# Optimization experiments

Measured on AMD Instinct MI355X. Metric: run time of the kernel, lower is better.

Reference implementation:

```python
import jax, jax.numpy as jnp
import numpy as np

N_LAYERS = 2
N_QUBITS = 2


def _ry(t):
    c, s = jnp.cos(t / 2), jnp.sin(t / 2)
    m = jnp.stack([jnp.stack([c, -s], -1), jnp.stack([s, c], -1)], -2)
    return m.astype(jnp.complex64)


def _rx(t):
    c = jnp.cos(t / 2).astype(jnp.complex64)
    s = (-1j) * jnp.sin(t / 2).astype(jnp.complex64)
    return jnp.stack([jnp.stack([c, s], -1), jnp.stack([s, c], -1)], -2)


def _rz(t):
    e = jnp.exp(-0.5j * t.astype(jnp.complex64))
    z = jnp.zeros_like(e)
    return jnp.stack([jnp.stack([e, z], -1), jnp.stack([z, jnp.conj(e)], -1)], -2)


def _apply_w0(G, s):
    # gate on wire 0 (most significant); s: [N,2,2] indexed [n, q0, q1]
    if G.ndim == 2:
        G = G[None]
    return jnp.matmul(G, s)


def _apply_w1(G, s):
    # gate on wire 1: contract last index with G
    if G.ndim == 2:
        G = G[None]
    return jnp.matmul(s, jnp.swapaxes(G, -1, -2))


def _qnn_batched(enc, qw):
    # enc: [N,2] float angles; qw: [2,2,3] trainable angles.
    # Batched 2-qubit statevector simulation, state shape [N,2,2] (q0,q1).
    N = enc.shape[0]
    s = jnp.zeros((N, 2, 2), jnp.complex64).at[:, 0, 0].set(1.0)
    # data encoding: RY(enc_i) on wire i
    s = _apply_w0(_ry(enc[:, 0]), s)
    s = _apply_w1(_ry(enc[:, 1]), s)
    for l in range(N_LAYERS):
        # RX then RY then RZ on each qubit => fused single-qubit gate RZ@RY@RX
        g0 = _rz(qw[l, 0, 2]) @ _ry(qw[l, 0, 1]) @ _rx(qw[l, 0, 0])
        g1 = _rz(qw[l, 1, 2]) @ _ry(qw[l, 1, 1]) @ _rx(qw[l, 1, 0])
        s = _apply_w0(g0, s)
        s = _apply_w1(g1, s)
        # CNOT(control=0, target=1): flip q1 where q0 == 1
        s = s.at[:, 1, :].set(s[:, 1, ::-1])
    p = (s * jnp.conj(s)).real  # probabilities [N,2,2]
    z0 = (p[:, 0, :] - p[:, 1, :]).sum(-1)
    z1 = (p[:, :, 0] - p[:, :, 1]).sum(-1)
    return jnp.stack([z0, z1], -1)  # [N,2]


def _mlp(x, w1, b1, w2, b2, w3, b3):
    h = jnp.tanh(x @ w1 + b1)
    h = jnp.tanh(h @ w2 + b2)
    return h @ w3 + b3


def setup_inputs() -> dict:
    key = jax.random.key(0)
    ks = jax.random.split(key, 15)
    N = 1_000_000
    W = 32

    def rn(k, shape, scale):
        return (scale * jax.random.normal(k, shape)).astype(jnp.float32)

    return {
        "x": rn(ks[0], (N, 1), 1.0),
        "pre_w1": rn(ks[1], (1, W), 1.0),
        "pre_b1": rn(ks[2], (W,), 0.1),
        "pre_w2": rn(ks[3], (W, W), 1.0 / np.sqrt(W)),
        "pre_b2": rn(ks[4], (W,), 0.1),
        "pre_w3": rn(ks[5], (W, 2), 1.0 / np.sqrt(W)),
        "pre_b3": rn(ks[6], (2,), 0.1),
        "q_weights": rn(ks[7], (N_LAYERS, N_QUBITS, 3), 0.1),
        "post_w1": rn(ks[8], (2, W), 1.0 / np.sqrt(2)),
        "post_b1": rn(ks[9], (W,), 0.1),
        "post_w2": rn(ks[10], (W, W), 1.0 / np.sqrt(W)),
        "post_b2": rn(ks[11], (W,), 0.1),
        "post_w3": rn(ks[12], (W, 1), 1.0 / np.sqrt(W)),
        "post_b3": rn(ks[13], (1,), 0.1),
    }


def reference(x, pre_w1, pre_b1, pre_w2, pre_b2, pre_w3, pre_b3, q_weights,
              post_w1, post_b1, post_w2, post_b2, post_w3, post_b3):
    q = _mlp(x, pre_w1, pre_b1, pre_w2, pre_b2, pre_w3, pre_b3)        # [N,2]
    qhat = _qnn_batched(q, q_weights)                                  # [N,2]
    u = _mlp(qhat, post_w1, post_b1, post_w2, post_b2, post_w3, post_b3)  # [N,1]
    return u
```

## Files before the change

kernel.cpp:

```cpp
#include <hip/hip_runtime.h>
#include <math.h>
#include <stdint.h>


typedef __attribute__((ext_vector_type(8))) short short8;
typedef __attribute__((ext_vector_type(4))) float f32x4;

union Frag { uint32_t u[4]; short8 s; };

__device__ __forceinline__ float fast_tanh(float x) {
    float e = __builtin_amdgcn_exp2f(x * 2.8853900817779268f);
    return fmaf(-2.0f, __builtin_amdgcn_rcpf(e + 1.0f), 1.0f);
}

__device__ __forceinline__ void split8(const float h[8], uint32_t hi[4], uint32_t lo[4]) {
    #pragma unroll
    for (int p = 0; p < 4; ++p) {
        uint32_t u0 = __float_as_uint(h[2*p])   & 0xFFFF0000u;
        uint32_t u1 = __float_as_uint(h[2*p+1]) & 0xFFFF0000u;
        float l0 = h[2*p]   - __uint_as_float(u0);
        float l1 = h[2*p+1] - __uint_as_float(u1);
        uint32_t v0 = __float_as_uint(l0) & 0xFFFF0000u;
        uint32_t v1 = __float_as_uint(l1) & 0xFFFF0000u;
        hi[p] = (u0 >> 16) | u1;
        lo[p] = (v0 >> 16) | v1;
    }
}

struct cplx { float re, im; };
__device__ __forceinline__ cplx cmul(cplx a, cplx b) {
    return { a.re * b.re - a.im * b.im, a.re * b.im + a.im * b.re };
}
__device__ __forceinline__ cplx cadd(cplx a, cplx b) {
    return { a.re + b.re, a.im + b.im };
}

__global__ void qcpinn_setup(const float* __restrict__ qw,
                             const float* __restrict__ pw2,
                             const float* __restrict__ ow2,
                             float* __restrict__ ws) {
    const int lane = threadIdx.x & 63;
    const int s = lane & 15, gg = lane >> 4;
    uint32_t* wsu = (uint32_t*)ws;

    #pragma unroll
    for (int m = 0; m < 2; ++m) {
        const float* W = m ? ow2 : pw2;
        #pragma unroll
        for (int r = 0; r < 2; ++r) {
            float v[8];
            #pragma unroll
            for (int j = 0; j < 8; ++j)
                v[j] = W[(gg * 8 + j) * 32 + (r * 16 + s)];
            uint32_t hi[4], lo[4];
            split8(v, hi, lo);
            int bh = 32 + ((m * 4 + r * 2 + 0) * 64 + lane) * 4;
            int bl = 32 + ((m * 4 + r * 2 + 1) * 64 + lane) * 4;
            #pragma unroll
            for (int p = 0; p < 4; ++p) { wsu[bh + p] = hi[p]; wsu[bl + p] = lo[p]; }
        }
    }

    if (threadIdx.x == 0) {
        cplx U[16];
        for (int i = 0; i < 16; ++i) U[i] = {0.f, 0.f};
        U[0].re = U[5].re = U[10].re = U[15].re = 1.f;

        for (int l = 0; l < 2; ++l) {
            cplx g[2][4];
            for (int w = 0; w < 2; ++w) {
                float a = qw[l * 6 + w * 3 + 0];
                float b = qw[l * 6 + w * 3 + 1];
                float c = qw[l * 6 + w * 3 + 2];
                float sa, ca, sb, cb, sc, cc;
                __sincosf(0.5f * a, &sa, &ca);
                __sincosf(0.5f * b, &sb, &cb);
                __sincosf(0.5f * c, &sc, &cc);
                cplx RX[4] = {{ca, 0.f}, {0.f, -sa}, {0.f, -sa}, {ca, 0.f}};
                cplx RY[4] = {{cb, 0.f}, {-sb, 0.f}, {sb, 0.f}, {cb, 0.f}};
                cplx RZ[4] = {{cc, -sc}, {0.f, 0.f}, {0.f, 0.f}, {cc, sc}};
                cplx T[4];
                for (int i2 = 0; i2 < 2; ++i2)
                    for (int j2 = 0; j2 < 2; ++j2) {
                        cplx acc = {0.f, 0.f};
                        for (int k2 = 0; k2 < 2; ++k2)
                            acc = cadd(acc, cmul(RY[i2 * 2 + k2], RX[k2 * 2 + j2]));
                        T[i2 * 2 + j2] = acc;
                    }
                for (int i2 = 0; i2 < 2; ++i2)
                    for (int j2 = 0; j2 < 2; ++j2) {
                        cplx acc = {0.f, 0.f};
                        for (int k2 = 0; k2 < 2; ++k2)
                            acc = cadd(acc, cmul(RZ[i2 * 2 + k2], T[k2 * 2 + j2]));
                        g[w][i2 * 2 + j2] = acc;
                    }
            }
            cplx L[16];
            for (int i4 = 0; i4 < 4; ++i4) {
                int si = (i4 == 2) ? 3 : (i4 == 3) ? 2 : i4;
                for (int j4 = 0; j4 < 4; ++j4)
                    L[i4 * 4 + j4] = cmul(g[1][(si & 1) * 2 + (j4 & 1)],
                                          g[0][(si >> 1) * 2 + (j4 >> 1)]);
            }
            cplx Un[16];
            for (int i4 = 0; i4 < 4; ++i4)
                for (int j4 = 0; j4 < 4; ++j4) {
                    cplx acc = {0.f, 0.f};
                    for (int k4 = 0; k4 < 4; ++k4)
                        acc = cadd(acc, cmul(L[i4 * 4 + k4], U[k4 * 4 + j4]));
                    Un[i4 * 4 + j4] = acc;
                }
            for (int i = 0; i < 16; ++i) U[i] = Un[i];
        }
        for (int i = 0; i < 16; ++i) { ws[i] = U[i].re; ws[16 + i] = U[i].im; }
    }
}

#define NT 4
__global__ __launch_bounds__(256, 4) void qcpinn_main(
    const float* __restrict__ x,
    const float* __restrict__ pw1, const float* __restrict__ pb1,
    const float* __restrict__ pb2, const float* __restrict__ pw3,
    const float* __restrict__ pb3,
    const float* __restrict__ ws,
    const float* __restrict__ ow1, const float* __restrict__ ob1,
    const float* __restrict__ ob2, const float* __restrict__ ow3,
    const float* __restrict__ ob3,
    float* __restrict__ out, int N)
{
    const int lane = threadIdx.x & 63;
    const int wid  = threadIdx.x >> 6;
    const int s    = lane & 15;
    const int g    = lane >> 4;
    const int base = (blockIdx.x * 4 + wid) * (NT * 16);

    const Frag* fragp = (const Frag*)(ws + 32);

    float xv[NT];
    #pragma unroll
    for (int t = 0; t < NT; ++t) {
        int idx = base + t * 16 + s;
        xv[t] = (idx < N) ? x[idx] : 0.f;
    }

    f32x4 w1a = *(const f32x4*)(pw1 + g * 8);
    f32x4 w1b = *(const f32x4*)(pw1 + g * 8 + 4);
    f32x4 b1a = *(const f32x4*)(pb1 + g * 8);
    f32x4 b1b = *(const f32x4*)(pb1 + g * 8 + 4);
    Frag A0h = fragp[0 * 64 + lane];
    Frag A0l = fragp[1 * 64 + lane];
    Frag A1h = fragp[2 * 64 + lane];
    Frag A1l = fragp[3 * 64 + lane];
    f32x4 pb2a = *(const f32x4*)(pb2 + g * 4);
    f32x4 pb2b = *(const f32x4*)(pb2 + 16 + g * 4);
    f32x4 w3a = *(const f32x4*)(pw3 + g * 8);
    f32x4 w3b = *(const f32x4*)(pw3 + g * 8 + 4);
    f32x4 w3c = *(const f32x4*)(pw3 + 32 + g * 8);
    f32x4 w3d = *(const f32x4*)(pw3 + 32 + g * 8 + 4);
    const float bq0 = pb3[0], bq1 = pb3[1];
    f32x4 Ure = *(const f32x4*)(ws + g * 4);
    f32x4 Uim = *(const f32x4*)(ws + 16 + g * 4);
    const float sgn0 = (g & 2) ? -1.f : 1.f;
    const float sgn1 = (g & 1) ? -1.f : 1.f;

    float z0[NT], z1[NT];
    #pragma unroll
    for (int t = 0; t < NT; ++t) {
        float h[8];
        #pragma unroll
        for (int j = 0; j < 4; ++j) {
            h[j]     = fast_tanh(fmaf(xv[t], w1a[j], b1a[j]));
            h[4 + j] = fast_tanh(fmaf(xv[t], w1b[j], b1b[j]));
        }
        Frag Bh, Bl;
        split8(h, Bh.u, Bl.u);

        f32x4 C0 = {0.f, 0.f, 0.f, 0.f};
        f32x4 C1 = {0.f, 0.f, 0.f, 0.f};
        C0 = __builtin_amdgcn_mfma_f32_16x16x32_bf16(A0h.s, Bh.s, C0, 0, 0, 0);
        C0 = __builtin_amdgcn_mfma_f32_16x16x32_bf16(A0h.s, Bl.s, C0, 0, 0, 0);
        C0 = __builtin_amdgcn_mfma_f32_16x16x32_bf16(A0l.s, Bh.s, C0, 0, 0, 0);
        C1 = __builtin_amdgcn_mfma_f32_16x16x32_bf16(A1h.s, Bh.s, C1, 0, 0, 0);
        C1 = __builtin_amdgcn_mfma_f32_16x16x32_bf16(A1h.s, Bl.s, C1, 0, 0, 0);
        C1 = __builtin_amdgcn_mfma_f32_16x16x32_bf16(A1l.s, Bh.s, C1, 0, 0, 0);

        float h2[8];
        #pragma unroll
        for (int i = 0; i < 4; ++i) {
            h2[i]     = fast_tanh(C0[i] + pb2a[i]);
            h2[4 + i] = fast_tanh(C1[i] + pb2b[i]);
        }

        float q0 = 0.f, q1 = 0.f;
        q0 = fmaf(h2[0], w3a[0], q0); q1 = fmaf(h2[0], w3a[1], q1);
        q0 = fmaf(h2[1], w3a[2], q0); q1 = fmaf(h2[1], w3a[3], q1);
        q0 = fmaf(h2[2], w3b[0], q0); q1 = fmaf(h2[2], w3b[1], q1);
        q0 = fmaf(h2[3], w3b[2], q0); q1 = fmaf(h2[3], w3b[3], q1);
        q0 = fmaf(h2[4], w3c[0], q0); q1 = fmaf(h2[4], w3c[1], q1);
        q0 = fmaf(h2[5], w3c[2], q0); q1 = fmaf(h2[5], w3c[3], q1);
        q0 = fmaf(h2[6], w3d[0], q0); q1 = fmaf(h2[6], w3d[1], q1);
        q0 = fmaf(h2[7], w3d[2], q0); q1 = fmaf(h2[7], w3d[3], q1);
        q0 += __shfl_xor(q0, 16); q0 += __shfl_xor(q0, 32); q0 += bq0;
        q1 += __shfl_xor(q1, 16); q1 += __shfl_xor(q1, 32); q1 += bq1;

        float s0, c0, s1, c1;
        __sincosf(0.5f * q0, &s0, &c0);
        __sincosf(0.5f * q1, &s1, &c1);
        float e0 = c0 * c1, e1 = c0 * s1, e2 = s0 * c1, e3 = s0 * s1;
        float re = fmaf(Ure[0], e0, fmaf(Ure[1], e1, fmaf(Ure[2], e2, Ure[3] * e3)));
        float im = fmaf(Uim[0], e0, fmaf(Uim[1], e1, fmaf(Uim[2], e2, Uim[3] * e3)));
        float p  = fmaf(re, re, im * im);
        float t0 = sgn0 * p, t1 = sgn1 * p;
        t0 += __shfl_xor(t0, 16); t0 += __shfl_xor(t0, 32);
        t1 += __shfl_xor(t1, 16); t1 += __shfl_xor(t1, 32);
        z0[t] = t0; z1[t] = t1;
    }

    f32x4 oa   = *(const f32x4*)(ow1 + g * 8);
    f32x4 oa2  = *(const f32x4*)(ow1 + g * 8 + 4);
    f32x4 obv  = *(const f32x4*)(ow1 + 32 + g * 8);
    f32x4 ob2v = *(const f32x4*)(ow1 + 32 + g * 8 + 4);
    f32x4 obb  = *(const f32x4*)(ob1 + g * 8);
    f32x4 obb2 = *(const f32x4*)(ob1 + g * 8 + 4);
    Frag P0h = fragp[4 * 64 + lane];
    Frag P0l = fragp[5 * 64 + lane];
    Frag P1h = fragp[6 * 64 + lane];
    Frag P1l = fragp[7 * 64 + lane];
    f32x4 ob2a = *(const f32x4*)(ob2 + g * 4);
    f32x4 ob2b = *(const f32x4*)(ob2 + 16 + g * 4);
    f32x4 w3o0 = *(const f32x4*)(ow3 + g * 4);
    f32x4 w3o1 = *(const f32x4*)(ow3 + 16 + g * 4);
    const float bo = ob3[0];

    #pragma unroll
    for (int t = 0; t < NT; ++t) {
        float h[8];
        #pragma unroll
        for (int j = 0; j < 4; ++j) {
            h[j]     = fast_tanh(fmaf(z0[t], oa[j],  fmaf(z1[t], obv[j],  obb[j])));
            h[4 + j] = fast_tanh(fmaf(z0[t], oa2[j], fmaf(z1[t], ob2v[j], obb2[j])));
        }
        Frag Bh, Bl;
        split8(h, Bh.u, Bl.u);

        f32x4 C0 = {0.f, 0.f, 0.f, 0.f};
        f32x4 C1 = {0.f, 0.f, 0.f, 0.f};
        C0 = __builtin_amdgcn_mfma_f32_16x16x32_bf16(P0h.s, Bh.s, C0, 0, 0, 0);
        C0 = __builtin_amdgcn_mfma_f32_16x16x32_bf16(P0h.s, Bl.s, C0, 0, 0, 0);
        C0 = __builtin_amdgcn_mfma_f32_16x16x32_bf16(P0l.s, Bh.s, C0, 0, 0, 0);
        C1 = __builtin_amdgcn_mfma_f32_16x16x32_bf16(P1h.s, Bh.s, C1, 0, 0, 0);
        C1 = __builtin_amdgcn_mfma_f32_16x16x32_bf16(P1h.s, Bl.s, C1, 0, 0, 0);
        C1 = __builtin_amdgcn_mfma_f32_16x16x32_bf16(P1l.s, Bh.s, C1, 0, 0, 0);

        float u = 0.f;
        #pragma unroll
        for (int i = 0; i < 4; ++i) {
            float ha = fast_tanh(C0[i] + ob2a[i]);
            float hb = fast_tanh(C1[i] + ob2b[i]);
            u = fmaf(ha, w3o0[i], u);
            u = fmaf(hb, w3o1[i], u);
        }
        u += __shfl_xor(u, 16);
        u += __shfl_xor(u, 32);
        u += bo;
        int idx = base + t * 16 + s;
        if (g == 0 && idx < N) out[idx] = u;
    }
}

extern "C" void kernel_launch(void* const* d_in, const int* in_sizes, int n_in,
                              void* d_out, int out_size, void* d_ws, size_t ws_size,
                              hipStream_t stream) {
    const float* x   = (const float*)d_in[0];
    const float* pw1 = (const float*)d_in[1];
    const float* pb1 = (const float*)d_in[2];
    const float* pw2 = (const float*)d_in[3];
    const float* pb2 = (const float*)d_in[4];
    const float* pw3 = (const float*)d_in[5];
    const float* pb3 = (const float*)d_in[6];
    const float* qw  = (const float*)d_in[7];
    const float* ow1 = (const float*)d_in[8];
    const float* ob1 = (const float*)d_in[9];
    const float* ow2 = (const float*)d_in[10];
    const float* ob2 = (const float*)d_in[11];
    const float* ow3 = (const float*)d_in[12];
    const float* ob3 = (const float*)d_in[13];
    float* out = (float*)d_out;
    float* ws  = (float*)d_ws;

    const int N = in_sizes[0];

    qcpinn_setup<<<1, 64, 0, stream>>>(qw, pw2, ow2, ws);

    const int grid = (N + 255) / 256;
    qcpinn_main<<<grid, 256, 0, stream>>>(
        x, pw1, pb1, pb2, pw3, pb3, ws,
        ow1, ob1, ob2, ow3, ob3, out, N);
}
```

Baseline: 126.3 us.

## Rewrite tanh as scaled sigmoid, fold constants into weights, stage params in LDS

Rewrites each tanh as 1-2*sigmoid and folds the scale factors, column sums and signs into the preprocessed weights and biases in the setup kernel. The main kernel then needs one exp and one rcp per activation with no extra FMA. The activation B operand drops from a hi/lo bf16 split to a single rounded bf16, which cuts MFMAs from 6 to 4 per layer and removes the split work. The two stages are fused into one loop. Parameters are staged through LDS, and the output store is coalesced so each lane writes one value. The cost is lower precision in the activations and an extra block-wide LDS copy and barrier.

New measurement: 118.8 us. 1.06x faster.

```diff
diff --git a/kernel.cpp b/kernel.cpp
--- a/kernel.cpp
+++ b/kernel.cpp
@@ -1,4 +1,5 @@
 #include <hip/hip_runtime.h>
+#include <hip/hip_bf16.h>
 #include <math.h>
 #include <stdint.h>
 
@@ -8,9 +9,30 @@
 
 union Frag { uint32_t u[4]; short8 s; };
 
-__device__ __forceinline__ float fast_tanh(float x) {
-    float e = __builtin_amdgcn_exp2f(x * 2.8853900817779268f);
-    return fmaf(-2.0f, __builtin_amdgcn_rcpf(e + 1.0f), 1.0f);
+#define KT 2.8853900817779268f
+
+#define L_FRAG 0
+#define L_U    2048
+#define L_W1   2080
+#define L_B1   2112
+#define L_BH2  2144
+#define L_W3   2176
+#define L_OW1  2240
+#define L_OB1  2304
+#define L_BH2P 2336
+#define L_OW3  2368
+#define L_SC   2400
+#define L_TOT  2416
+
+__device__ __forceinline__ float sig_act(float y) {
+    return __builtin_amdgcn_rcpf(__builtin_amdgcn_exp2f(y) + 1.0f);
+}
+
+__device__ __forceinline__ uint32_t pk_bf16(float a, float b) {
+    union { __hip_bfloat162 h; uint32_t u; } cv;
+    cv.h.x = __float2bfloat16(a);
+    cv.h.y = __float2bfloat16(b);
+    return cv.u;
 }
 
 __device__ __forceinline__ void split8(const float h[8], uint32_t hi[4], uint32_t lo[4]) {
@@ -35,10 +57,16 @@
     return { a.re + b.re, a.im + b.im };
 }
 
-__global__ void qcpinn_setup(const float* __restrict__ qw,
-                             const float* __restrict__ pw2,
-                             const float* __restrict__ ow2,
-                             float* __restrict__ ws) {
+__global__ void qcpinn_setup(
+    const float* __restrict__ pw1, const float* __restrict__ pb1,
+    const float* __restrict__ pw2, const float* __restrict__ pb2,
+    const float* __restrict__ pw3, const float* __restrict__ pb3,
+    const float* __restrict__ qw,
+    const float* __restrict__ ow1, const float* __restrict__ ob1,
+    const float* __restrict__ ow2, const float* __restrict__ ob2,
+    const float* __restrict__ ow3, const float* __restrict__ ob3,
+    float* __restrict__ ws)
+{
     const int lane = threadIdx.x & 63;
     const int s = lane & 15, gg = lane >> 4;
     uint32_t* wsu = (uint32_t*)ws;
@@ -51,21 +79,47 @@
             float v[8];
             #pragma unroll
             for (int j = 0; j < 8; ++j)
-                v[j] = W[(gg * 8 + j) * 32 + (r * 16 + s)];
+                v[j] = -2.0f * KT * W[(gg * 8 + j) * 32 + (r * 16 + s)];
             uint32_t hi[4], lo[4];
             split8(v, hi, lo);
-            int bh = 32 + ((m * 4 + r * 2 + 0) * 64 + lane) * 4;
-            int bl = 32 + ((m * 4 + r * 2 + 1) * 64 + lane) * 4;
+            int bh = L_FRAG + ((m * 4 + r * 2 + 0) * 256) + lane * 4;
+            int bl = L_FRAG + ((m * 4 + r * 2 + 1) * 256) + lane * 4;
             #pragma unroll
             for (int p = 0; p < 4; ++p) { wsu[bh + p] = hi[p]; wsu[bl + p] = lo[p]; }
         }
     }
 
-    if (threadIdx.x == 0) {
+    if (lane < 32) {
+        int j = lane;
+        float cs_p = 0.f, cs_o = 0.f;
+        for (int k = 0; k < 32; ++k) { cs_p += pw2[k * 32 + j]; cs_o += ow2[k * 32 + j]; }
+        ws[L_W1 + j]   = KT * pw1[j];
+        ws[L_B1 + j]   = KT * pb1[j];
+        ws[L_BH2 + j]  = KT * (pb2[j] + cs_p);
+        ws[L_OB1 + j]  = KT * ob1[j];
+        ws[L_BH2P + j] = KT * (ob2[j] + cs_o);
+        ws[L_OW3 + j]  = -2.f * ow3[j];
+        ws[L_W3 + j * 2]     = -pw3[j * 2];
+        ws[L_W3 + j * 2 + 1] = -pw3[j * 2 + 1];
+        float sg0 = (j & 16) ? -1.f : 1.f;
+        float sg1 = (j & 8)  ? -1.f : 1.f;
+        ws[L_OW1 + j]      = KT * sg0 * ow1[j];
+        ws[L_OW1 + 32 + j] = KT * sg1 * ow1[32 + j];
+    }
+
+    if (lane == 0) {
+        float cw0 = 0.f, cw1 = 0.f, co3 = 0.f;
+        for (int k = 0; k < 32; ++k) {
+            cw0 += pw3[k * 2]; cw1 += pw3[k * 2 + 1]; co3 += ow3[k];
+        }
+        ws[L_SC + 0] = 0.5f * (pb3[0] + cw0);
+        ws[L_SC + 1] = 0.5f * (pb3[1] + cw1);
+        ws[L_SC + 2] = ob3[0] + co3;
+        ws[L_SC + 3] = 0.f;
+
         cplx U[16];
         for (int i = 0; i < 16; ++i) U[i] = {0.f, 0.f};
         U[0].re = U[5].re = U[10].re = U[15].re = 1.f;
-
         for (int l = 0; l < 2; ++l) {
             cplx g[2][4];
             for (int w = 0; w < 2; ++w) {
@@ -112,29 +166,30 @@
                 }
             for (int i = 0; i < 16; ++i) U[i] = Un[i];
         }
-        for (int i = 0; i < 16; ++i) { ws[i] = U[i].re; ws[16 + i] = U[i].im; }
+        for (int i = 0; i < 16; ++i) { ws[L_U + i] = U[i].re; ws[L_U + 16 + i] = U[i].im; }
     }
 }
 
 #define NT 4
-__global__ __launch_bounds__(256, 4) void qcpinn_main(
-    const float* __restrict__ x,
-    const float* __restrict__ pw1, const float* __restrict__ pb1,
-    const float* __restrict__ pb2, const float* __restrict__ pw3,
-    const float* __restrict__ pb3,
-    const float* __restrict__ ws,
-    const float* __restrict__ ow1, const float* __restrict__ ob1,
-    const float* __restrict__ ob2, const float* __restrict__ ow3,
-    const float* __restrict__ ob3,
+__global__ __launch_bounds__(256) void qcpinn_main(
+    const float* __restrict__ x, const float* __restrict__ ws,
     float* __restrict__ out, int N)
 {
+    __shared__ float lds[L_TOT];
+    {
+        const float4* src = (const float4*)ws;
+        float4* dst = (float4*)lds;
+        for (int i = threadIdx.x; i < L_TOT / 4; i += 256) dst[i] = src[i];
+    }
+    __syncthreads();
+
     const int lane = threadIdx.x & 63;
     const int wid  = threadIdx.x >> 6;
     const int s    = lane & 15;
     const int g    = lane >> 4;
-    const int base = (blockIdx.x * 4 + wid) * (NT * 16);
-
-    const Frag* fragp = (const Frag*)(ws + 32);
+    const int base = (blockIdx.x * 4 + wid) * 64;
+
+    const Frag* frag = (const Frag*)(lds + L_FRAG);
 
     float xv[NT];
     #pragma unroll
@@ -143,129 +198,113 @@
         xv[t] = (idx < N) ? x[idx] : 0.f;
     }
 
-    f32x4 w1a = *(const f32x4*)(pw1 + g * 8);
-    f32x4 w1b = *(const f32x4*)(pw1 + g * 8 + 4);
-    f32x4 b1a = *(const f32x4*)(pb1 + g * 8);
-    f32x4 b1b = *(const f32x4*)(pb1 + g * 8 + 4);
-    Frag A0h = fragp[0 * 64 + lane];
-    Frag A0l = fragp[1 * 64 + lane];
-    Frag A1h = fragp[2 * 64 + lane];
-    Frag A1l = fragp[3 * 64 + lane];
-    f32x4 pb2a = *(const f32x4*)(pb2 + g * 4);
-    f32x4 pb2b = *(const f32x4*)(pb2 + 16 + g * 4);
-    f32x4 w3a = *(const f32x4*)(pw3 + g * 8);
-    f32x4 w3b = *(const f32x4*)(pw3 + g * 8 + 4);
-    f32x4 w3c = *(const f32x4*)(pw3 + 32 + g * 8);
-    f32x4 w3d = *(const f32x4*)(pw3 + 32 + g * 8 + 4);
-    const float bq0 = pb3[0], bq1 = pb3[1];
-    f32x4 Ure = *(const f32x4*)(ws + g * 4);
-    f32x4 Uim = *(const f32x4*)(ws + 16 + g * 4);
-    const float sgn0 = (g & 2) ? -1.f : 1.f;
-    const float sgn1 = (g & 1) ? -1.f : 1.f;
-
-    float z0[NT], z1[NT];
+    f32x4 w1a = *(const f32x4*)(lds + L_W1 + g * 8);
+    f32x4 w1b = *(const f32x4*)(lds + L_W1 + g * 8 + 4);
+    f32x4 b1a = *(const f32x4*)(lds + L_B1 + g * 8);
+    f32x4 b1b = *(const f32x4*)(lds + L_B1 + g * 8 + 4);
+    Frag A0h = frag[0 * 64 + lane], A0l = frag[1 * 64 + lane];
+    Frag A1h = frag[2 * 64 + lane], A1l = frag[3 * 64 + lane];
+    f32x4 bh2a = *(const f32x4*)(lds + L_BH2 + g * 4);
+    f32x4 bh2b = *(const f32x4*)(lds + L_BH2 + 16 + g * 4);
+    f32x4 w3a = *(const f32x4*)(lds + L_W3 + g * 8);
+    f32x4 w3b = *(const f32x4*)(lds + L_W3 + g * 8 + 4);
+    f32x4 w3c = *(const f32x4*)(lds + L_W3 + 32 + g * 8);
+    f32x4 w3d = *(const f32x4*)(lds + L_W3 + 32 + g * 8 + 4);
+    f32x4 Ure = *(const f32x4*)(lds + L_U + g * 4);
+    f32x4 Uim = *(const f32x4*)(lds + L_U + 16 + g * 4);
+    const float qb0 = lds[L_SC + 0], qb1 = lds[L_SC + 1], bo = lds[L_SC + 2];
+    f32x4 oa   = *(const f32x4*)(lds + L_OW1 + g * 8);
+    f32x4 oa2  = *(const f32x4*)(lds + L_OW1 + g * 8 + 4);
+    f32x4 obv  = *(const f32x4*)(lds + L_OW1 + 32 + g * 8);
+    f32x4 ob2v = *(const f32x4*)(lds + L_OW1 + 32 + g * 8 + 4);
+    f32x4 obb  = *(const f32x4*)(lds + L_OB1 + g * 8);
+    f32x4 obb2 = *(const f32x4*)(lds + L_OB1 + g * 8 + 4);
+    Frag P0h = frag[4 * 64 + lane], P0l = frag[5 * 64 + lane];
+    Frag P1h = frag[6 * 64 + lane], P1l = frag[7 * 64 + lane];
+    f32x4 bpa = *(const f32x4*)(lds + L_BH2P + g * 4);
+    f32x4 bpb = *(const f32x4*)(lds + L_BH2P + 16 + g * 4);
+    f32x4 w3o0 = *(const f32x4*)(lds + L_OW3 + g * 4);
+    f32x4 w3o1 = *(const f32x4*)(lds + L_OW3 + 16 + g * 4);
+
+    float uo[NT];
     #pragma unroll
     for (int t = 0; t < NT; ++t) {
-        float h[8];
+        float r1[8];
         #pragma unroll
         for (int j = 0; j < 4; ++j) {
-            h[j]     = fast_tanh(fmaf(xv[t], w1a[j], b1a[j]));
-            h[4 + j] = fast_tanh(fmaf(xv[t], w1b[j], b1b[j]));
-        }
-        Frag Bh, Bl;
-        split8(h, Bh.u, Bl.u);
-
-        f32x4 C0 = {0.f, 0.f, 0.f, 0.f};
-        f32x4 C1 = {0.f, 0.f, 0.f, 0.f};
-        C0 = __builtin_amdgcn_mfma_f32_16x16x32_bf16(A0h.s, Bh.s, C0, 0, 0, 0);
-        C0 = __builtin_amdgcn_mfma_f32_16x16x32_bf16(A0h.s, Bl.s, C0, 0, 0, 0);
-        C0 = __builtin_amdgcn_mfma_f32_16x16x32_bf16(A0l.s, Bh.s, C0, 0, 0, 0);
-        C1 = __builtin_amdgcn_mfma_f32_16x16x32_bf16(A1h.s, Bh.s, C1, 0, 0, 0);
-        C1 = __builtin_amdgcn_mfma_f32_16x16x32_bf16(A1h.s, Bl.s, C1, 0, 0, 0);
-        C1 = __builtin_amdgcn_mfma_f32_16x16x32_bf16(A1l.s, Bh.s, C1, 0, 0, 0);
-
-        float h2[8];
-        #pragma unroll
-        for (int i = 0; i < 4; ++i) {
-            h2[i]     = fast_tanh(C0[i] + pb2a[i]);
-            h2[4 + i] = fast_tanh(C1[i] + pb2b[i]);
-        }
-
-        float q0 = 0.f, q1 = 0.f;
-        q0 = fmaf(h2[0], w3a[0], q0); q1 = fmaf(h2[0], w3a[1], q1);
-        q0 = fmaf(h2[1], w3a[2], q0); q1 = fmaf(h2[1], w3a[3], q1);
-        q0 = fmaf(h2[2], w3b[0], q0); q1 = fmaf(h2[2], w3b[1], q1);
-        q0 = fmaf(h2[3], w3b[2], q0); q1 = fmaf(h2[3], w3b[3], q1);
-        q0 = fmaf(h2[4], w3c[0], q0); q1 = fmaf(h2[4], w3c[1], q1);
-        q0 = fmaf(h2[5], w3c[2], q0); q1 = fmaf(h2[5], w3c[3], q1);
-        q0 = fmaf(h2[6], w3d[0], q0); q1 = fmaf(h2[6], w3d[1], q1);
-        q0 = fmaf(h2[7], w3d[2], q0); q1 = fmaf(h2[7], w3d[3], q1);
-        q0 += __shfl_xor(q0, 16); q0 += __shfl_xor(q0, 32); q0 += bq0;
-        q1 += __shfl_xor(q1, 16); q1 += __shfl_xor(q1, 32); q1 += bq1;
+            r1[j]     = sig_act(fmaf(xv[t], w1a[j], b1a[j]));
+            r1[4 + j] = sig_act(fmaf(xv[t], w1b[j], b1b[j]));
+        }
+        Frag B;
+        #pragma unroll
+        for (int p = 0; p < 4; ++p) B.u[p] = pk_bf16(r1[2*p], r1[2*p+1]);
+
+        f32x4 C0 = bh2a, C1 = bh2b;
+        C0 = __builtin_amdgcn_mfma_f32_16x16x32_bf16(A0h.s, B.s, C0, 0, 0, 0);
+        C0 = __builtin_amdgcn_mfma_f32_16x16x32_bf16(A0l.s, B.s, C0, 0, 0, 0);
+        C1 = __builtin_amdgcn_mfma_f32_16x16x32_bf16(A1h.s, B.s, C1, 0, 0, 0);
+        C1 = __builtin_amdgcn_mfma_f32_16x16x32_bf16(A1l.s, B.s, C1, 0, 0, 0);
+        float r2[8];
+        #pragma unroll
+        for (int i = 0; i < 4; ++i) { r2[i] = sig_act(C0[i]); r2[4+i] = sig_act(C1[i]); }
+
+        float q0, q1;
+        q0 = r2[0] * w3a[0];           q1 = r2[0] * w3a[1];
+        q0 = fmaf(r2[1], w3a[2], q0);  q1 = fmaf(r2[1], w3a[3], q1);
+        q0 = fmaf(r2[2], w3b[0], q0);  q1 = fmaf(r2[2], w3b[1], q1);
+        q0 = fmaf(r2[3], w3b[2], q0);  q1 = fmaf(r2[3], w3b[3], q1);
+        q0 = fmaf(r2[4], w3c[0], q0);  q1 = fmaf(r2[4], w3c[1], q1);
+        q0 = fmaf(r2[5], w3c[2], q0);  q1 = fmaf(r2[5], w3c[3], q1);
+        q0 = fmaf(r2[6], w3d[0], q0);  q1 = fmaf(r2[6], w3d[1], q1);
+        q0 = fmaf(r2[7], w3d[2], q0);  q1 = fmaf(r2[7], w3d[3], q1);
+        q0 += __shfl_xor(q0, 16); q0 += __shfl_xor(q0, 32); q0 += qb0;
+        q1 += __shfl_xor(q1, 16); q1 += __shfl_xor(q1, 32); q1 += qb1;
 
         float s0, c0, s1, c1;
-        __sincosf(0.5f * q0, &s0, &c0);
-        __sincosf(0.5f * q1, &s1, &c1);
+        __sincosf(q0, &s0, &c0);
+        __sincosf(q1, &s1, &c1);
         float e0 = c0 * c1, e1 = c0 * s1, e2 = s0 * c1, e3 = s0 * s1;
         float re = fmaf(Ure[0], e0, fmaf(Ure[1], e1, fmaf(Ure[2], e2, Ure[3] * e3)));
         float im = fmaf(Uim[0], e0, fmaf(Uim[1], e1, fmaf(Uim[2], e2, Uim[3] * e3)));
         float p  = fmaf(re, re, im * im);
-        float t0 = sgn0 * p, t1 = sgn1 * p;
-        t0 += __shfl_xor(t0, 16); t0 += __shfl_xor(t0, 32);
-        t1 += __shfl_xor(t1, 16); t1 += __shfl_xor(t1, 32);
-        z0[t] = t0; z1[t] = t1;
-    }
-
-    f32x4 oa   = *(const f32x4*)(ow1 + g * 8);
-    f32x4 oa2  = *(const f32x4*)(ow1 + g * 8 + 4);
-    f32x4 obv  = *(const f32x4*)(ow1 + 32 + g * 8);
-    f32x4 ob2v = *(const f32x4*)(ow1 + 32 + g * 8 + 4);
-    f32x4 obb  = *(const f32x4*)(ob1 + g * 8);
-    f32x4 obb2 = *(const f32x4*)(ob1 + g * 8 + 4);
-    Frag P0h = fragp[4 * 64 + lane];
-    Frag P0l = fragp[5 * 64 + lane];
-    Frag P1h = fragp[6 * 64 + lane];
-    Frag P1l = fragp[7 * 64 + lane];
-    f32x4 ob2a = *(const f32x4*)(ob2 + g * 4);
-    f32x4 ob2b = *(const f32x4*)(ob2 + 16 + g * 4);
-    f32x4 w3o0 = *(const f32x4*)(ow3 + g * 4);
-    f32x4 w3o1 = *(const f32x4*)(ow3 + 16 + g * 4);
-    const float bo = ob3[0];
-
-    #pragma unroll
-    for (int t = 0; t < NT; ++t) {
-        float h[8];
+
+        float pr   = __shfl_xor(p, 16);
+        float sm   = p + pr, df = p - pr;
+        float z0pm = sm - __shfl_xor(sm, 32);
+        float z1pm = df + __shfl_xor(df, 32);
+
+        float r3[8];
         #pragma unroll
         for (int j = 0; j < 4; ++j) {
-            h[j]     = fast_tanh(fmaf(z0[t], oa[j],  fmaf(z1[t], obv[j],  obb[j])));
-            h[4 + j] = fast_tanh(fmaf(z0[t], oa2[j], fmaf(z1[t], ob2v[j], obb2[j])));
-        }
-        Frag Bh, Bl;
-        split8(h, Bh.u, Bl.u);
-
-        f32x4 C0 = {0.f, 0.f, 0.f, 0.f};
-        f32x4 C1 = {0.f, 0.f, 0.f, 0.f};
-        C0 = __builtin_amdgcn_mfma_f32_16x16x32_bf16(P0h.s, Bh.s, C0, 0, 0, 0);
-        C0 = __builtin_amdgcn_mfma_f32_16x16x32_bf16(P0h.s, Bl.s, C0, 0, 0, 0);
-        C0 = __builtin_amdgcn_mfma_f32_16x16x32_bf16(P0l.s, Bh.s, C0, 0, 0, 0);
-        C1 = __builtin_amdgcn_mfma_f32_16x16x32_bf16(P1h.s, Bh.s, C1, 0, 0, 0);
-        C1 = __builtin_amdgcn_mfma_f32_16x16x32_bf16(P1h.s, Bl.s, C1, 0, 0, 0);
-        C1 = __builtin_amdgcn_mfma_f32_16x16x32_bf16(P1l.s, Bh.s, C1, 0, 0, 0);
+            r3[j]     = sig_act(fmaf(z0pm, oa[j],  fmaf(z1pm, obv[j],  obb[j])));
+            r3[4 + j] = sig_act(fmaf(z0pm, oa2[j], fmaf(z1pm, ob2v[j], obb2[j])));
+        }
+        Frag B2;
+        #pragma unroll
+        for (int p2 = 0; p2 < 4; ++p2) B2.u[p2] = pk_bf16(r3[2*p2], r3[2*p2+1]);
+
+        f32x4 D0 = bpa, D1 = bpb;
+        D0 = __builtin_amdgcn_mfma_f32_16x16x32_bf16(P0h.s, B2.s, D0, 0, 0, 0);
+        D0 = __builtin_amdgcn_mfma_f32_16x16x32_bf16(P0l.s, B2.s, D0, 0, 0, 0);
+        D1 = __builtin_amdgcn_mfma_f32_16x16x32_bf16(P1h.s, B2.s, D1, 0, 0, 0);
+        D1 = __builtin_amdgcn_mfma_f32_16x16x32_bf16(P1l.s, B2.s, D1, 0, 0, 0);
 
         float u = 0.f;
         #pragma unroll
         for (int i = 0; i < 4; ++i) {
-            float ha = fast_tanh(C0[i] + ob2a[i]);
-            float hb = fast_tanh(C1[i] + ob2b[i]);
-            u = fmaf(ha, w3o0[i], u);
-            u = fmaf(hb, w3o1[i], u);
+            u = fmaf(sig_act(D0[i]), w3o0[i], u);
+            u = fmaf(sig_act(D1[i]), w3o1[i], u);
         }
         u += __shfl_xor(u, 16);
         u += __shfl_xor(u, 32);
-        u += bo;
-        int idx = base + t * 16 + s;
-        if (g == 0 && idx < N) out[idx] = u;
-    }
+        uo[t] = u;
+    }
+
+    float ua = (g & 1) ? uo[1] : uo[0];
+    float ub = (g & 1) ? uo[3] : uo[2];
+    float us = ((g & 2) ? ub : ua) + bo;
+    int oidx = base + lane;
+    if (oidx < N) out[oidx] = us;
 }
 
 extern "C" void kernel_launch(void* const* d_in, const int* in_sizes, int n_in,
@@ -290,10 +329,9 @@
 
     const int N = in_sizes[0];
 
-    qcpinn_setup<<<1, 64, 0, stream>>>(qw, pw2, ow2, ws);
+    qcpinn_setup<<<1, 64, 0, stream>>>(pw1, pb1, pw2, pb2, pw3, pb3, qw,
+                                       ow1, ob1, ow2, ob2, ow3, ob3, ws);
 
     const int grid = (N + 255) / 256;
-    qcpinn_main<<<grid, 256, 0, stream>>>(
-        x, pw1, pb1, pb2, pw3, pb3, ws,
-        ow1, ob1, ob2, ow3, ob3, out, N);
-}
+    qcpinn_main<<<grid, 256, 0, stream>>>(x, ws, out, N);
+}
```
